# Performance work log

Hardware: AMD Instinct MI355X
Metric: run time of the kernel (lower is better)

Reference implementation:

```python
import jax, jax.numpy as jnp
import numpy as np

N = 20000      # total atoms
M = 12         # neighbors per atom
B = 41         # nbr_fea_len
ORIG = 92      # orig_atom_fea_len
F = 64         # atom_fea_len
D = 2 * F + B  # 169, gated feature width
NC = 3         # n_conv
K = 3          # k parallel gates per conv
H = 128        # h_fea_len
N0 = 400       # crystals in batch
EPS = 1e-5     # batchnorm eps


def setup_inputs() -> dict:
    key = jax.random.key(0)
    ks = jax.random.split(key, 24)
    inp = {}
    inp["atom_fea"] = jax.random.normal(ks[0], (N, ORIG), jnp.float32)
    inp["nbr_fea"] = jax.random.normal(ks[1], (N, M, B), jnp.float32)
    inp["nbr_fea_idx"] = jax.random.randint(ks[2], (N, M), 0, N)
    inp["crystal_atom_idx"] = jnp.sort(jax.random.randint(ks[3], (N,), 0, N0))
    inp["n_crystals"] = N0
    inp["emb_w"] = jax.random.normal(ks[4], (ORIG, F)) * 0.1
    inp["emb_b"] = jnp.zeros((F,), jnp.float32)
    inp["fc_w"] = jax.random.normal(ks[5], (NC, K, D, D)) * 0.05
    inp["fc_b"] = jnp.zeros((NC, K, D), jnp.float32)
    inp["bn1_g"] = jnp.ones((NC, K, D), jnp.float32)
    inp["bn1_b"] = jnp.zeros((NC, K, D), jnp.float32)
    inp["bn1_m"] = jax.random.normal(ks[6], (NC, K, D)) * 0.1
    inp["bn1_v"] = jax.random.uniform(ks[7], (NC, K, D)) * 0.5 + 0.75
    inp["bn2_g"] = jnp.ones((NC, K, F), jnp.float32)
    inp["bn2_b"] = jnp.zeros((NC, K, F), jnp.float32)
    inp["bn2_m"] = jax.random.normal(ks[8], (NC, K, F)) * 0.1
    inp["bn2_v"] = jax.random.uniform(ks[9], (NC, K, F)) * 0.5 + 0.75
    inp["atom_w"] = jax.random.normal(ks[10], (NC, K, 2 * K)) * 0.3
    inp["atom_b"] = jnp.zeros((NC, 2 * K), jnp.float32)
    inp["nbr_w"] = jax.random.normal(ks[11], (NC, K, 2 * K)) * 0.3
    inp["nbr_b"] = jnp.zeros((NC, 2 * K), jnp.float32)
    inp["fc1_w"] = jax.random.normal(ks[12], (F, H)) * 0.1
    inp["fc1_b"] = jnp.zeros((H,), jnp.float32)
    inp["out_w"] = jax.random.normal(ks[13], (H, 1)) * 0.1
    inp["out_b"] = jnp.zeros((1,), jnp.float32)
    return inp


def _conv(atom_in, nbr, idx, fc_w, fc_b, bn1_g, bn1_b, bn1_m, bn1_v,
          bn2_g, bn2_b, bn2_m, bn2_v, atom_w, atom_b, nbr_w, nbr_b):
    n, m = idx.shape
    gathered = atom_in[idx]                                   # (N,M,F) irregular gather
    self_f = jnp.broadcast_to(atom_in[:, None, :], (n, m, F))
    total = jnp.concatenate([self_f, gathered, nbr], axis=2)  # (N,M,D)
    # k parallel linear layers, vectorized over k
    g = jnp.einsum('nmd,kde->knme', total, fc_w) + fc_b[:, None, None, :]  # (K,N,M,D)
    # bn1 (eval mode, running stats)
    g = (g - bn1_m[:, None, None, :]) * jax.lax.rsqrt(bn1_v[:, None, None, :] + EPS) \
        * bn1_g[:, None, None, :] + bn1_b[:, None, None, :]
    nbr_filter = jax.nn.softmax(g[..., :F], axis=2)            # softmax over neighbors M
    nbr_core = jax.nn.relu(g[..., F:2 * F])
    new_nbr_k = g[..., 2 * F:] + nbr[None]                     # (K,N,M,B) residual on bonds
    summed = jnp.sum(nbr_filter * nbr_core, axis=2)            # (K,N,F)
    summed = (summed - bn2_m[:, None, :]) * jax.lax.rsqrt(bn2_v[:, None, :] + EPS) \
        * bn2_g[:, None, :] + bn2_b[:, None, :]
    out_k = atom_in[None] + summed                             # (K,N,F) residual on atoms
    out = jnp.moveaxis(out_k, 0, 2)                            # (N,F,K)
    new_nbr = jnp.moveaxis(new_nbr_k, 0, 3)                    # (N,M,B,K)
    og = out @ atom_w + atom_b                                 # (N,F,2K)
    ng = new_nbr @ nbr_w + nbr_b                               # (N,M,B,2K)
    out = jnp.sum(og[..., :K] * jax.nn.softmax(og[..., K:], axis=2), axis=2)
    new_nbr = jnp.sum(ng[..., :K] * jax.nn.softmax(ng[..., K:], axis=3), axis=3)
    return out, new_nbr


def reference(atom_fea, nbr_fea, nbr_fea_idx, crystal_atom_idx, n_crystals,
              emb_w, emb_b, fc_w, fc_b, bn1_g, bn1_b, bn1_m, bn1_v,
              bn2_g, bn2_b, bn2_m, bn2_v, atom_w, atom_b, nbr_w, nbr_b,
              fc1_w, fc1_b, out_w, out_b):
    x = atom_fea @ emb_w + emb_b                               # embedding
    nbr = nbr_fea
    for i in range(NC):                                        # fixed small layer loop
        x, nbr = _conv(x, nbr, nbr_fea_idx,
                       fc_w[i], fc_b[i], bn1_g[i], bn1_b[i], bn1_m[i], bn1_v[i],
                       bn2_g[i], bn2_b[i], bn2_m[i], bn2_v[i],
                       atom_w[i], atom_b[i], nbr_w[i], nbr_b[i])
    # per-crystal mean pooling via segment sum
    sums = jax.ops.segment_sum(x, crystal_atom_idx, num_segments=n_crystals)
    counts = jax.ops.segment_sum(jnp.ones((x.shape[0], 1), x.dtype),
                                 crystal_atom_idx, num_segments=n_crystals)
    crys = sums / jnp.maximum(counts, 1.0)
    crys = jax.nn.relu(crys) @ fc1_w + fc1_b
    crys = jax.nn.relu(crys)
    return crys @ out_w + out_b                                # (N0, 1)
```

## Files before the change

kernel.cpp:

```cpp
#include <hip/hip_runtime.h>
#include <math.h>

#define N_ATOMS 20000
#define M 12
#define B 41
#define ORIG 92
#define F 64
#define D 169
#define NCONV 3
#define K 3
#define TWOK 6
#define H 128
#define N0 400
#define EPS 1e-5f
#define KB (K * B)
#define NBRS 42

#define KPAD 192
#define NS 6
#define ATOMS_PER_BLK 4
#define ROWS (ATOMS_PER_BLK * 16)
#define THREADS 512
#define LFRAG 98304
#define WT_USHORTS (NCONV * 2 * LFRAG)
#define GRID (N_ATOMS / ATOMS_PER_BLK)

typedef __attribute__((ext_vector_type(8))) short bf16x8;
typedef __attribute__((ext_vector_type(4))) float f32x4;

__device__ inline unsigned short f32_to_bf16(float v) {
    unsigned int x = __float_as_uint(v);
    unsigned int r = (x + 0x7fffu + ((x >> 16) & 1u)) >> 16;
    return (unsigned short)r;
}
__device__ inline float bf16_to_f32(unsigned short u) {
    return __uint_as_float(((unsigned int)u) << 16);
}
__device__ inline unsigned int pack_hilo(float v) {
    unsigned short hi = f32_to_bf16(v);
    unsigned short lo = f32_to_bf16(v - bf16_to_f32(hi));
    return (unsigned int)hi | ((unsigned int)lo << 16);
}
__device__ inline float unpack_hilo(unsigned int p) {
    return bf16_to_f32((unsigned short)(p & 0xFFFFu)) +
           bf16_to_f32((unsigned short)(p >> 16));
}

__global__ void emb_kernel(const float* __restrict__ atom_fea,
                           const float* __restrict__ emb_w,
                           const float* __restrict__ emb_b,
                           float* __restrict__ x,
                           unsigned int* __restrict__ xp) {
    int i = blockIdx.x * blockDim.x + threadIdx.x;
    if (i >= N_ATOMS * F) return;
    int n = i / F, f = i % F;
    const float* a = atom_fea + n * ORIG;
    float acc = emb_b[f];
    #pragma unroll 4
    for (int d = 0; d < ORIG; ++d)
        acc = fmaf(a[d], emb_w[d * F + f], acc);
    x[i] = acc;
    xp[i] = pack_hilo(acc);
}

__global__ void npack_kernel(const float* __restrict__ nbr_fea,
                             unsigned int* __restrict__ nbrp) {
    int i = blockIdx.x * blockDim.x + threadIdx.x;
    if (i >= N_ATOMS * M * NBRS) return;
    int nm = i / NBRS, slot = i - nm * NBRS;
    nbrp[i] = (slot < B) ? pack_hilo(nbr_fea[nm * B + slot]) : 0u;
}

__global__ void prep_kernel(const float* __restrict__ fc_w,
                            unsigned short* __restrict__ wt) {
    int i = blockIdx.x * blockDim.x + threadIdx.x;
    if (i >= NCONV * LFRAG) return;
    int layer = i / LFRAG;
    int r = i % LFRAG;
    int s = r / 16384;
    int r2 = r % 16384;
    int c16 = r2 / 512;
    int r3 = r2 % 512;
    int lane = r3 / 8;
    int e = r3 % 8;
    int col = c16 * 16 + (lane & 15);
    int k = s * 32 + (lane >> 4) * 8 + e;
    float v = 0.f;
    if (k < D) {
        int b3 = col >> 7, cc = col & 127;
        if (b3 < 3) {
            v = fc_w[((size_t)(layer * K + b3) * D + k) * D + cc];
        } else if (cc < KB) {
            int kk = cc / B, bb = cc - kk * B;
            v = fc_w[((size_t)(layer * K + kk) * D + k) * D + 2 * F + bb];
        }
    }
    unsigned short hi = f32_to_bf16(v);
    float hf = bf16_to_f32(hi);
    unsigned short lo = f32_to_bf16(v - hf);
    size_t off = (size_t)s * 16384 + c16 * 512 + lane * 8 + e;
    wt[(size_t)(layer * 2 + 0) * LFRAG + off] = hi;
    wt[(size_t)(layer * 2 + 1) * LFRAG + off] = lo;
}

__global__ void prep2_kernel(const float* __restrict__ fc_b,
                             const float* __restrict__ bn1_g,
                             const float* __restrict__ bn1_b,
                             const float* __restrict__ bn1_m,
                             const float* __restrict__ bn1_v,
                             const float* __restrict__ bn2_g,
                             const float* __restrict__ bn2_b,
                             const float* __restrict__ bn2_m,
                             const float* __restrict__ bn2_v,
                             float* __restrict__ sc1,
                             float* __restrict__ sh1,
                             float* __restrict__ sc2,
                             float* __restrict__ sh2) {
    int i = blockIdx.x * blockDim.x + threadIdx.x;
    if (i < NCONV * K * D) {
        float sc = bn1_g[i] * rsqrtf(bn1_v[i] + EPS);
        sc1[i] = sc;
        sh1[i] = fmaf(fc_b[i], sc, bn1_b[i] - bn1_m[i] * sc);
    }
    if (i < NCONV * K * F) {
        float sc = bn2_g[i] * rsqrtf(bn2_v[i] + EPS);
        sc2[i] = sc;
        sh2[i] = bn2_b[i] - bn2_m[i] * sc;
    }
}

template <bool NEED_NBR>
__global__ __launch_bounds__(THREADS, 4)
void conv_mfma(const float* __restrict__ xin,
               const unsigned int* __restrict__ xpin,
               const unsigned int* __restrict__ nbrpin,
               const int* __restrict__ idx,
               const unsigned short* __restrict__ wtl,
               const float* __restrict__ sc1,
               const float* __restrict__ sh1,
               const float* __restrict__ sc2,
               const float* __restrict__ sh2,
               const float* __restrict__ atom_w,
               const float* __restrict__ atom_b,
               const float* __restrict__ nbr_w,
               const float* __restrict__ nbr_b,
               float* __restrict__ xout,
               unsigned int* __restrict__ xpout,
               unsigned int* __restrict__ nbrpout) {
    __shared__ unsigned short s_a[2 * ROWS * KPAD];
    __shared__ float s_sum[ATOMS_PER_BLK * K * F];

    const int t = threadIdx.x;
    const int w = t >> 6;
    const int l = t & 63;
    const int l15 = l & 15;
    const int lane3 = l >> 4;
    const int n0 = blockIdx.x * ATOMS_PER_BLK;

    {
        const int srow = t >> 3;
        const int j8 = t & 7;
        const int a = srow >> 4, m = srow & 15;
        const int n = n0 + a;
        const unsigned int mask = (unsigned int)((srow & 7) << 4);
        char* hi_base = (char*)s_a + srow * (KPAD * 2);
        char* lo_base = hi_base + 2 * ROWS * KPAD;
        if (m < M) {
            const unsigned int* xs = xpin + n * F;
            const unsigned int* xg = xpin + idx[n * M + m] * F;
            const unsigned int* nb = nbrpin + (size_t)(n * M + m) * NBRS;
            #pragma unroll
            for (int q = 0; q < 12; ++q) {
                int kp = j8 + 8 * q;
                uint2 u;
                if (kp < 32)       u = *(const uint2*)&xs[kp * 2];
                else if (kp < 64)  u = *(const uint2*)&xg[kp * 2 - 64];
                else if (kp < 85)  u = *(const uint2*)&nb[kp * 2 - 128];
                else               u = make_uint2(0u, 0u);
                unsigned int hip = (u.x & 0xFFFFu) | (u.y << 16);
                unsigned int lop = (u.x >> 16) | (u.y & 0xFFFF0000u);
                unsigned int byo = ((unsigned int)(kp * 4)) ^ mask;
                *(unsigned int*)(hi_base + byo) = hip;
                *(unsigned int*)(lo_base + byo) = lop;
            }
        } else {
            #pragma unroll
            for (int q = 0; q < 12; ++q) {
                unsigned int byo = ((unsigned int)((j8 + 8 * q) * 4)) ^ mask;
                *(unsigned int*)(hi_base + byo) = 0u;
                *(unsigned int*)(lo_base + byo) = 0u;
            }
        }
    }
    __syncthreads();

    const int kk_gate = w >> 1, half = w & 1;
    int tile[4];
    if (w < 6) {
        tile[0] = kk_gate * 8 + half * 2 + 0;
        tile[1] = kk_gate * 8 + half * 2 + 1;
        tile[2] = tile[0] + 4;
        tile[3] = tile[1] + 4;
    } else {
        tile[0] = 24 + (w - 6) * 4 + 0;
        tile[1] = 24 + (w - 6) * 4 + 1;
        tile[2] = 24 + (w - 6) * 4 + 2;
        tile[3] = 24 + (w - 6) * 4 + 3;
    }

    f32x4 acc[ATOMS_PER_BLK][4];
    #pragma unroll
    for (int a = 0; a < ATOMS_PER_BLK; ++a)
        #pragma unroll
        for (int j = 0; j < 4; ++j)
            acc[a][j] = (f32x4){0.f, 0.f, 0.f, 0.f};

    if (!(w >= 6 && !NEED_NBR)) {
        __builtin_amdgcn_s_setprio(1);
        for (int s = 0; s < NS; ++s) {
            bf16x8 ah[ATOMS_PER_BLK], al[ATOMS_PER_BLK];
            #pragma unroll
            for (int a = 0; a < ATOMS_PER_BLK; ++a) {
                int row = a * 16 + l15;
                int koff = s * 64 + lane3 * 16;
                int byte = row * (KPAD * 2) + (koff ^ ((row & 7) << 4));
                ah[a] = *reinterpret_cast<const bf16x8*>(&s_a[byte >> 1]);
                al[a] = *reinterpret_cast<const bf16x8*>(&s_a[(byte >> 1) + ROWS * KPAD]);
            }
            #pragma unroll
            for (int j = 0; j < 4; ++j) {
                const unsigned short* wp =
                    wtl + (size_t)s * 16384 + tile[j] * 512 + l * 8;
                bf16x8 bh = *reinterpret_cast<const bf16x8*>(wp);
                bf16x8 bl = *reinterpret_cast<const bf16x8*>(wp + LFRAG);
                #pragma unroll
                for (int a = 0; a < ATOMS_PER_BLK; ++a) {
                    acc[a][j] = __builtin_amdgcn_mfma_f32_16x16x32_bf16(ah[a], bh, acc[a][j], 0, 0, 0);
                    acc[a][j] = __builtin_amdgcn_mfma_f32_16x16x32_bf16(ah[a], bl, acc[a][j], 0, 0, 0);
                    acc[a][j] = __builtin_amdgcn_mfma_f32_16x16x32_bf16(al[a], bh, acc[a][j], 0, 0, 0);
                }
            }
        }
        __builtin_amdgcn_s_setprio(0);
    }
    __syncthreads();

    float* s_nnk = reinterpret_cast<float*>(s_a);

    if (w < 6) {
        const int k = kk_gate;
        #pragma unroll
        for (int a = 0; a < ATOMS_PER_BLK; ++a) {
            #pragma unroll
            for (int j = 0; j < 2; ++j) {
                int e = (half * 2 + j) * 16 + l15;
                int cf = k * D + e, cr = cf + F, c2 = k * F + e;
                float sc_f = sc1[cf], sh_f = sh1[cf];
                float sc_c = sc1[cr], sh_c = sh1[cr];
                bool act = (lane3 < 3);
                float fv[4], cv[4];
                #pragma unroll
                for (int r = 0; r < 4; ++r) {
                    fv[r] = fmaf(acc[a][j][r], sc_f, sh_f);
                    cv[r] = fmaxf(fmaf(acc[a][j + 2][r], sc_c, sh_c), 0.f);
                }
                float mx = act ? fmaxf(fmaxf(fv[0], fv[1]), fmaxf(fv[2], fv[3])) : -1e30f;
                mx = fmaxf(mx, __shfl_xor(mx, 16));
                mx = fmaxf(mx, __shfl_xor(mx, 32));
                float se = 0.f, sp = 0.f;
                #pragma unroll
                for (int r = 0; r < 4; ++r) {
                    float ex = act ? __expf(fv[r] - mx) : 0.f;
                    se += ex;
                    sp = fmaf(ex, cv[r], sp);
                }
                se += __shfl_xor(se, 16);
                se += __shfl_xor(se, 32);
                sp += __shfl_xor(sp, 16);
                sp += __shfl_xor(sp, 32);
                float summed = sp / se;
                float outv = xin[(n0 + a) * F + e] + fmaf(summed, sc2[c2], sh2[c2]);
                if (lane3 == 0) s_sum[(a * K + k) * F + e] = outv;
            }
        }
    } else if (NEED_NBR) {
        #pragma unroll
        for (int a = 0; a < ATOMS_PER_BLK; ++a) {
            #pragma unroll
            for (int j = 0; j < 4; ++j) {
                int cc = (w - 6) * 64 + j * 16 + l15;
                if (cc < KB) {
                    int kk = cc / B, bb = cc - (cc / B) * B;
                    int col = kk * D + 2 * F + bb;
                    float sc = sc1[col], sh = sh1[col];
                    #pragma unroll
                    for (int r = 0; r < 4; ++r) {
                        int m = lane3 * 4 + r;
                        if (m < M) {
                            float nv = unpack_hilo(
                                nbrpin[(size_t)((n0 + a) * M + m) * NBRS + bb]);
                            s_nnk[((a * K + kk) * M + m) * B + bb] =
                                fmaf(acc[a][j][r], sc, sh) + nv;
                        }
                    }
                }
            }
        }
    }
    __syncthreads();

    if (t < ATOMS_PER_BLK * F) {
        int a2 = t >> 6, f = t & 63;
        float og[TWOK];
        #pragma unroll
        for (int j = 0; j < TWOK; ++j) {
            float v = atom_b[j];
            #pragma unroll
            for (int q = 0; q < K; ++q)
                v = fmaf(s_sum[(a2 * K + q) * F + f], atom_w[q * TWOK + j], v);
            og[j] = v;
        }
        float mx = fmaxf(fmaxf(og[K], og[K + 1]), og[K + 2]);
        float e0 = __expf(og[K] - mx), e1 = __expf(og[K + 1] - mx), e2 = __expf(og[K + 2] - mx);
        float inv = 1.f / (e0 + e1 + e2);
        float outv = (og[0] * e0 + og[1] * e1 + og[2] * e2) * inv;
        xout[(n0 + a2) * F + f] = outv;
        xpout[(n0 + a2) * F + f] = pack_hilo(outv);
    }

    if (NEED_NBR) {
        for (int i = t; i < ATOMS_PER_BLK * M * B; i += THREADS) {
            int a2 = i / (M * B);
            int r = i - a2 * (M * B);
            int m = r / B, b = r - m * B;
            float ng[TWOK];
            #pragma unroll
            for (int j = 0; j < TWOK; ++j) {
                float v = nbr_b[j];
                #pragma unroll
                for (int q = 0; q < K; ++q)
                    v = fmaf(s_nnk[((a2 * K + q) * M + m) * B + b], nbr_w[q * TWOK + j], v);
                ng[j] = v;
            }
            float mx = fmaxf(fmaxf(ng[K], ng[K + 1]), ng[K + 2]);
            float e0 = __expf(ng[K] - mx), e1 = __expf(ng[K + 1] - mx), e2 = __expf(ng[K + 2] - mx);
            float inv = 1.f / (e0 + e1 + e2);
            float v = (ng[0] * e0 + ng[1] * e1 + ng[2] * e2) * inv;
            nbrpout[(size_t)((n0 + a2) * M + m) * NBRS + b] = pack_hilo(v);
        }
        for (int i3 = t; i3 < ATOMS_PER_BLK * M; i3 += THREADS) {
            int a2 = i3 / M, m = i3 - a2 * M;
            nbrpout[(size_t)((n0 + a2) * M + m) * NBRS + B] = 0u;
        }
    }
}

__global__ void pool_kernel(const float* __restrict__ x,
                            const int* __restrict__ cidx,
                            float* __restrict__ sums,
                            float* __restrict__ cnt) {
    int i = blockIdx.x * blockDim.x + threadIdx.x;
    if (i >= N_ATOMS * F) return;
    int n = i / F, f = i % F;
    int c = cidx[n];
    atomicAdd(&sums[c * F + f], x[i]);
    if (f == 0) atomicAdd(&cnt[c], 1.0f);
}

__global__ void head_kernel(const float* __restrict__ sums,
                            const float* __restrict__ cnt,
                            const float* __restrict__ fc1_w,
                            const float* __restrict__ fc1_b,
                            const float* __restrict__ out_w,
                            const float* __restrict__ out_b,
                            float* __restrict__ out) {
    const int c = blockIdx.x;
    const int t = threadIdx.x;
    __shared__ float a[F];
    __shared__ float red[H];
    float inv_cnt = 1.f / fmaxf(cnt[c], 1.0f);
    if (t < F) a[t] = fmaxf(sums[c * F + t] * inv_cnt, 0.f);
    __syncthreads();
    float hv = fc1_b[t];
    #pragma unroll 4
    for (int f = 0; f < F; ++f)
        hv = fmaf(a[f], fc1_w[f * H + t], hv);
    hv = fmaxf(hv, 0.f);
    red[t] = hv * out_w[t];
    __syncthreads();
    for (int s = H / 2; s > 0; s >>= 1) {
        if (t < s) red[t] += red[t + s];
        __syncthreads();
    }
    if (t == 0) out[c] = red[0] + out_b[0];
}

extern "C" void kernel_launch(void* const* d_in, const int* in_sizes, int n_in,
                              void* d_out, int out_size, void* d_ws, size_t ws_size,
                              hipStream_t stream) {
    (void)in_sizes; (void)n_in; (void)out_size; (void)ws_size;
    const float* atom_fea = (const float*)d_in[0];
    const float* nbr_fea  = (const float*)d_in[1];
    const int*   nbr_idx  = (const int*)d_in[2];
    const int*   cidx     = (const int*)d_in[3];
    const float* emb_w = (const float*)d_in[5];
    const float* emb_b = (const float*)d_in[6];
    const float* fc_w  = (const float*)d_in[7];
    const float* fc_b  = (const float*)d_in[8];
    const float* bn1_g = (const float*)d_in[9];
    const float* bn1_b = (const float*)d_in[10];
    const float* bn1_m = (const float*)d_in[11];
    const float* bn1_v = (const float*)d_in[12];
    const float* bn2_g = (const float*)d_in[13];
    const float* bn2_b = (const float*)d_in[14];
    const float* bn2_m = (const float*)d_in[15];
    const float* bn2_v = (const float*)d_in[16];
    const float* atom_w = (const float*)d_in[17];
    const float* atom_b = (const float*)d_in[18];
    const float* nbr_w  = (const float*)d_in[19];
    const float* nbr_b  = (const float*)d_in[20];
    const float* fc1_w  = (const float*)d_in[21];
    const float* fc1_b  = (const float*)d_in[22];
    const float* out_w  = (const float*)d_in[23];
    const float* out_b  = (const float*)d_in[24];
    float* out = (float*)d_out;

    float* xA   = (float*)d_ws;
    float* xB   = xA + (size_t)N_ATOMS * F;
    unsigned int* xPA = (unsigned int*)(xB + (size_t)N_ATOMS * F);
    unsigned int* xPB = xPA + (size_t)N_ATOMS * F;
    unsigned int* nbrP0 = xPB + (size_t)N_ATOMS * F;
    unsigned int* nbrPA = nbrP0 + (size_t)N_ATOMS * M * NBRS;
    float* sums = (float*)(nbrPA + (size_t)N_ATOMS * M * NBRS);
    float* cnt  = sums + (size_t)N0 * F;
    float* sc1  = cnt + N0;
    float* sh1  = sc1 + NCONV * K * D;
    float* sc2  = sh1 + NCONV * K * D;
    float* sh2  = sc2 + NCONV * K * F;
    unsigned short* wt = (unsigned short*)(sh2 + NCONV * K * F);

    prep_kernel<<<(NCONV * LFRAG + 255) / 256, 256, 0, stream>>>(fc_w, wt);
    prep2_kernel<<<(NCONV * K * D + 255) / 256, 256, 0, stream>>>(
        fc_b, bn1_g, bn1_b, bn1_m, bn1_v, bn2_g, bn2_b, bn2_m, bn2_v,
        sc1, sh1, sc2, sh2);
    npack_kernel<<<(N_ATOMS * M * NBRS + 255) / 256, 256, 0, stream>>>(nbr_fea, nbrP0);
    emb_kernel<<<(N_ATOMS * F + 255) / 256, 256, 0, stream>>>(
        atom_fea, emb_w, emb_b, xA, xPA);

    conv_mfma<true><<<GRID, THREADS, 0, stream>>>(
        xA, xPA, nbrP0, nbr_idx,
        wt, sc1, sh1, sc2, sh2,
        atom_w, atom_b, nbr_w, nbr_b, xB, xPB, nbrPA);
    conv_mfma<true><<<GRID, THREADS, 0, stream>>>(
        xB, xPB, nbrPA, nbr_idx,
        wt + (size_t)2 * LFRAG,
        sc1 + (size_t)1 * K * D, sh1 + (size_t)1 * K * D,
        sc2 + (size_t)1 * K * F, sh2 + (size_t)1 * K * F,
        atom_w + (size_t)1 * K * TWOK, atom_b + (size_t)1 * TWOK,
        nbr_w + (size_t)1 * K * TWOK, nbr_b + (size_t)1 * TWOK, xA, xPA, nbrP0);
    conv_mfma<false><<<GRID, THREADS, 0, stream>>>(
        xA, xPA, nbrP0, nbr_idx,
        wt + (size_t)4 * LFRAG,
        sc1 + (size_t)2 * K * D, sh1 + (size_t)2 * K * D,
        sc2 + (size_t)2 * K * F, sh2 + (size_t)2 * K * F,
        atom_w + (size_t)2 * K * TWOK, atom_b + (size_t)2 * TWOK,
        nbr_w + (size_t)2 * K * TWOK, nbr_b + (size_t)2 * TWOK, xB, xPB, nbrPA);

    hipMemsetAsync(sums, 0, (size_t)(N0 * F + N0) * sizeof(float), stream);
    pool_kernel<<<(N_ATOMS * F + 255) / 256, 256, 0, stream>>>(xB, cidx, sums, cnt);
    head_kernel<<<N0, H, 0, stream>>>(sums, cnt, fc1_w, fc1_b, out_w, out_b, out);
}
```

Measured before the change: 620.1 us.

## Precompute self-atom GEMM contribution per atom instead of per neighbor

Splits the gated linear layer so the self-feature part (first 64 input rows) is computed once per atom in a new pw_kernel and stored as a per-atom 512-wide buffer. The conv kernel then only multiplies the gathered neighbor and bond features (K reduced from 192 to 128) and adds the precomputed partial sums in the epilogue. This removes redundant 12x recomputation of the self term and shrinks shared memory staging. In exchange it adds an extra kernel launch per layer and writes and reads a 20000x512 float buffer, about 40 MB per layer.

```diff
diff --git a/kernel.cpp b/kernel.cpp
--- a/kernel.cpp
+++ b/kernel.cpp
@@ -16,13 +16,13 @@
 #define KB (K * B)
 #define NBRS 42
 
-#define KPAD 192
-#define NS 6
+#define KPAD 128
+#define NS 4
 #define ATOMS_PER_BLK 4
 #define ROWS (ATOMS_PER_BLK * 16)
 #define THREADS 512
-#define LFRAG 98304
-#define WT_USHORTS (NCONV * 2 * LFRAG)
+#define LFRAG_C 65536
+#define LFRAG_P 32768
 #define GRID (N_ATOMS / ATOMS_PER_BLK)
 
 typedef __attribute__((ext_vector_type(8))) short bf16x8;
@@ -44,6 +44,17 @@
 __device__ inline float unpack_hilo(unsigned int p) {
     return bf16_to_f32((unsigned short)(p & 0xFFFFu)) +
            bf16_to_f32((unsigned short)(p >> 16));
+}
+
+__device__ inline float wlookup(const float* __restrict__ fc_w,
+                                int layer, int row, int c) {
+    int b3 = c >> 7, cc = c & 127;
+    if (b3 < 3) return fc_w[((size_t)(layer * K + b3) * D + row) * D + cc];
+    if (cc < KB) {
+        int kk = cc / B, bb = cc - (cc / B) * B;
+        return fc_w[((size_t)(layer * K + kk) * D + row) * D + 2 * F + bb];
+    }
+    return 0.f;
 }
 
 __global__ void emb_kernel(const float* __restrict__ atom_fea,
@@ -71,36 +82,44 @@
     nbrp[i] = (slot < B) ? pack_hilo(nbr_fea[nm * B + slot]) : 0u;
 }
 
-__global__ void prep_kernel(const float* __restrict__ fc_w,
-                            unsigned short* __restrict__ wt) {
+__global__ void prep_c_kernel(const float* __restrict__ fc_w,
+                              unsigned short* __restrict__ wt) {
     int i = blockIdx.x * blockDim.x + threadIdx.x;
-    if (i >= NCONV * LFRAG) return;
-    int layer = i / LFRAG;
-    int r = i % LFRAG;
+    if (i >= NCONV * LFRAG_C) return;
+    int layer = i / LFRAG_C;
+    int r = i % LFRAG_C;
     int s = r / 16384;
     int r2 = r % 16384;
     int c16 = r2 / 512;
     int r3 = r2 % 512;
-    int lane = r3 / 8;
-    int e = r3 % 8;
+    int lane = r3 / 8, e = r3 % 8;
+    int col = c16 * 16 + (lane & 15);
+    int k = 64 + s * 32 + (lane >> 4) * 8 + e;
+    float v = (k < D) ? wlookup(fc_w, layer, k, col) : 0.f;
+    unsigned short hi = f32_to_bf16(v);
+    unsigned short lo = f32_to_bf16(v - bf16_to_f32(hi));
+    wt[(size_t)(layer * 2 + 0) * LFRAG_C + r] = hi;
+    wt[(size_t)(layer * 2 + 1) * LFRAG_C + r] = lo;
+}
+
+__global__ void prep_p_kernel(const float* __restrict__ fc_w,
+                              unsigned short* __restrict__ wt) {
+    int i = blockIdx.x * blockDim.x + threadIdx.x;
+    if (i >= NCONV * LFRAG_P) return;
+    int layer = i / LFRAG_P;
+    int r = i % LFRAG_P;
+    int s = r / 16384;
+    int r2 = r % 16384;
+    int c16 = r2 / 512;
+    int r3 = r2 % 512;
+    int lane = r3 / 8, e = r3 % 8;
     int col = c16 * 16 + (lane & 15);
     int k = s * 32 + (lane >> 4) * 8 + e;
-    float v = 0.f;
-    if (k < D) {
-        int b3 = col >> 7, cc = col & 127;
-        if (b3 < 3) {
-            v = fc_w[((size_t)(layer * K + b3) * D + k) * D + cc];
-        } else if (cc < KB) {
-            int kk = cc / B, bb = cc - kk * B;
-            v = fc_w[((size_t)(layer * K + kk) * D + k) * D + 2 * F + bb];
-        }
-    }
+    float v = wlookup(fc_w, layer, k, col);
     unsigned short hi = f32_to_bf16(v);
-    float hf = bf16_to_f32(hi);
-    unsigned short lo = f32_to_bf16(v - hf);
-    size_t off = (size_t)s * 16384 + c16 * 512 + lane * 8 + e;
-    wt[(size_t)(layer * 2 + 0) * LFRAG + off] = hi;
-    wt[(size_t)(layer * 2 + 1) * LFRAG + off] = lo;
+    unsigned short lo = f32_to_bf16(v - bf16_to_f32(hi));
+    wt[(size_t)(layer * 2 + 0) * LFRAG_P + r] = hi;
+    wt[(size_t)(layer * 2 + 1) * LFRAG_P + r] = lo;
 }
 
 __global__ void prep2_kernel(const float* __restrict__ fc_b,
@@ -129,6 +148,78 @@
     }
 }
 
+__global__ __launch_bounds__(512, 4)
+void pw_kernel(const unsigned int* __restrict__ xp,
+               const unsigned short* __restrict__ wtl,
+               float* __restrict__ pw) {
+    __shared__ __align__(16) unsigned short s_a[2 * 32 * 64];
+
+    const int t = threadIdx.x;
+    const int w = t >> 6, l = t & 63;
+    const int l15 = l & 15, lane3 = l >> 4;
+    const int n0 = blockIdx.x * 32;
+
+    {
+        int row = t >> 4, j16 = t & 15;
+        unsigned int mask = (unsigned int)((row & 7) << 4);
+        char* hb = (char*)s_a + row * 128;
+        const unsigned int* xr = xp + (n0 + row) * F;
+        #pragma unroll
+        for (int q = 0; q < 2; ++q) {
+            int kp = j16 + 16 * q;
+            uint2 u = *(const uint2*)&xr[kp * 2];
+            unsigned int hip = (u.x & 0xFFFFu) | (u.y << 16);
+            unsigned int lop = (u.x >> 16) | (u.y & 0xFFFF0000u);
+            unsigned int byo = ((unsigned int)(kp * 4)) ^ mask;
+            *(unsigned int*)(hb + byo) = hip;
+            *(unsigned int*)(hb + byo + 4096) = lop;
+        }
+    }
+    __syncthreads();
+
+    f32x4 acc[2][4];
+    #pragma unroll
+    for (int a = 0; a < 2; ++a)
+        #pragma unroll
+        for (int j = 0; j < 4; ++j)
+            acc[a][j] = (f32x4){0.f, 0.f, 0.f, 0.f};
+
+    #pragma unroll
+    for (int s = 0; s < 2; ++s) {
+        bf16x8 ah[2], al[2];
+        #pragma unroll
+        for (int a = 0; a < 2; ++a) {
+            int row = a * 16 + l15;
+            int byte = row * 128 + ((s * 64 + lane3 * 16) ^ ((row & 7) << 4));
+            ah[a] = *(const bf16x8*)((const char*)s_a + byte);
+            al[a] = *(const bf16x8*)((const char*)s_a + byte + 4096);
+        }
+        #pragma unroll
+        for (int j = 0; j < 4; ++j) {
+            const unsigned short* wp = wtl + s * 16384 + (w * 4 + j) * 512 + l * 8;
+            bf16x8 bh = *(const bf16x8*)wp;
+            bf16x8 bl = *(const bf16x8*)(wp + LFRAG_P);
+            #pragma unroll
+            for (int a = 0; a < 2; ++a) {
+                acc[a][j] = __builtin_amdgcn_mfma_f32_16x16x32_bf16(ah[a], bh, acc[a][j], 0, 0, 0);
+                acc[a][j] = __builtin_amdgcn_mfma_f32_16x16x32_bf16(ah[a], bl, acc[a][j], 0, 0, 0);
+                acc[a][j] = __builtin_amdgcn_mfma_f32_16x16x32_bf16(al[a], bh, acc[a][j], 0, 0, 0);
+            }
+        }
+    }
+
+    #pragma unroll
+    for (int a = 0; a < 2; ++a)
+        #pragma unroll
+        for (int j = 0; j < 4; ++j) {
+            int col = (w * 4 + j) * 16 + l15;
+            int rowb = n0 + a * 16 + lane3 * 4;
+            #pragma unroll
+            for (int r = 0; r < 4; ++r)
+                pw[(size_t)(rowb + r) * 512 + col] = acc[a][j][r];
+        }
+}
+
 template <bool NEED_NBR>
 __global__ __launch_bounds__(THREADS, 4)
 void conv_mfma(const float* __restrict__ xin,
@@ -136,6 +227,7 @@
                const unsigned int* __restrict__ nbrpin,
                const int* __restrict__ idx,
                const unsigned short* __restrict__ wtl,
+               const float* __restrict__ pw,
                const float* __restrict__ sc1,
                const float* __restrict__ sh1,
                const float* __restrict__ sc2,
@@ -166,16 +258,14 @@
         char* hi_base = (char*)s_a + srow * (KPAD * 2);
         char* lo_base = hi_base + 2 * ROWS * KPAD;
         if (m < M) {
-            const unsigned int* xs = xpin + n * F;
             const unsigned int* xg = xpin + idx[n * M + m] * F;
             const unsigned int* nb = nbrpin + (size_t)(n * M + m) * NBRS;
             #pragma unroll
-            for (int q = 0; q < 12; ++q) {
+            for (int q = 0; q < 8; ++q) {
                 int kp = j8 + 8 * q;
                 uint2 u;
-                if (kp < 32)       u = *(const uint2*)&xs[kp * 2];
-                else if (kp < 64)  u = *(const uint2*)&xg[kp * 2 - 64];
-                else if (kp < 85)  u = *(const uint2*)&nb[kp * 2 - 128];
+                if (kp < 32)       u = *(const uint2*)&xg[kp * 2];
+                else if (kp < 53)  u = *(const uint2*)&nb[(kp - 32) * 2];
                 else               u = make_uint2(0u, 0u);
                 unsigned int hip = (u.x & 0xFFFFu) | (u.y << 16);
                 unsigned int lop = (u.x >> 16) | (u.y & 0xFFFF0000u);
@@ -185,7 +275,7 @@
             }
         } else {
             #pragma unroll
-            for (int q = 0; q < 12; ++q) {
+            for (int q = 0; q < 8; ++q) {
                 unsigned int byo = ((unsigned int)((j8 + 8 * q) * 4)) ^ mask;
                 *(unsigned int*)(hi_base + byo) = 0u;
                 *(unsigned int*)(lo_base + byo) = 0u;
@@ -232,7 +322,7 @@
                 const unsigned short* wp =
                     wtl + (size_t)s * 16384 + tile[j] * 512 + l * 8;
                 bf16x8 bh = *reinterpret_cast<const bf16x8*>(wp);
-                bf16x8 bl = *reinterpret_cast<const bf16x8*>(wp + LFRAG);
+                bf16x8 bl = *reinterpret_cast<const bf16x8*>(wp + LFRAG_C);
                 #pragma unroll
                 for (int a = 0; a < ATOMS_PER_BLK; ++a) {
                     acc[a][j] = __builtin_amdgcn_mfma_f32_16x16x32_bf16(ah[a], bh, acc[a][j], 0, 0, 0);
@@ -251,9 +341,13 @@
         const int k = kk_gate;
         #pragma unroll
         for (int a = 0; a < ATOMS_PER_BLK; ++a) {
+            const float* pwl = pw + (size_t)(n0 + a) * 512;
             #pragma unroll
             for (int j = 0; j < 2; ++j) {
                 int e = (half * 2 + j) * 16 + l15;
+                int colf = tile[j] * 16 + l15;
+                float Pf = pwl[colf];
+                float Pc = pwl[colf + 64];
                 int cf = k * D + e, cr = cf + F, c2 = k * F + e;
                 float sc_f = sc1[cf], sh_f = sh1[cf];
                 float sc_c = sc1[cr], sh_c = sh1[cr];
@@ -261,8 +355,8 @@
                 float fv[4], cv[4];
                 #pragma unroll
                 for (int r = 0; r < 4; ++r) {
-                    fv[r] = fmaf(acc[a][j][r], sc_f, sh_f);
-                    cv[r] = fmaxf(fmaf(acc[a][j + 2][r], sc_c, sh_c), 0.f);
+                    fv[r] = fmaf(acc[a][j][r] + Pf, sc_f, sh_f);
+                    cv[r] = fmaxf(fmaf(acc[a][j + 2][r] + Pc, sc_c, sh_c), 0.f);
                 }
                 float mx = act ? fmaxf(fmaxf(fv[0], fv[1]), fmaxf(fv[2], fv[3])) : -1e30f;
                 mx = fmaxf(mx, __shfl_xor(mx, 16));
@@ -286,10 +380,12 @@
     } else if (NEED_NBR) {
         #pragma unroll
         for (int a = 0; a < ATOMS_PER_BLK; ++a) {
+            const float* pwl = pw + (size_t)(n0 + a) * 512;
             #pragma unroll
             for (int j = 0; j < 4; ++j) {
                 int cc = (w - 6) * 64 + j * 16 + l15;
                 if (cc < KB) {
+                    float P1 = pwl[384 + cc];
                     int kk = cc / B, bb = cc - (cc / B) * B;
                     int col = kk * D + 2 * F + bb;
                     float sc = sc1[col], sh = sh1[col];
@@ -300,7 +396,7 @@
                             float nv = unpack_hilo(
                                 nbrpin[(size_t)((n0 + a) * M + m) * NBRS + bb]);
                             s_nnk[((a * K + kk) * M + m) * B + bb] =
-                                fmaf(acc[a][j][r], sc, sh) + nv;
+                                fmaf(acc[a][j][r] + P1, sc, sh) + nv;
                         }
                     }
                 }
@@ -431,15 +527,18 @@
     unsigned int* xPB = xPA + (size_t)N_ATOMS * F;
     unsigned int* nbrP0 = xPB + (size_t)N_ATOMS * F;
     unsigned int* nbrPA = nbrP0 + (size_t)N_ATOMS * M * NBRS;
-    float* sums = (float*)(nbrPA + (size_t)N_ATOMS * M * NBRS);
+    float* pwbuf = (float*)(nbrPA + (size_t)N_ATOMS * M * NBRS);
+    float* sums = pwbuf + (size_t)N_ATOMS * 512;
     float* cnt  = sums + (size_t)N0 * F;
     float* sc1  = cnt + N0;
     float* sh1  = sc1 + NCONV * K * D;
     float* sc2  = sh1 + NCONV * K * D;
     float* sh2  = sc2 + NCONV * K * F;
-    unsigned short* wt = (unsigned short*)(sh2 + NCONV * K * F);
-
-    prep_kernel<<<(NCONV * LFRAG + 255) / 256, 256, 0, stream>>>(fc_w, wt);
+    unsigned short* wtp = (unsigned short*)(sh2 + NCONV * K * F);
+    unsigned short* wtc = wtp + (size_t)NCONV * 2 * LFRAG_P;
+
+    prep_p_kernel<<<(NCONV * LFRAG_P + 255) / 256, 256, 0, stream>>>(fc_w, wtp);
+    prep_c_kernel<<<(NCONV * LFRAG_C + 255) / 256, 256, 0, stream>>>(fc_w, wtc);
     prep2_kernel<<<(NCONV * K * D + 255) / 256, 256, 0, stream>>>(
         fc_b, bn1_g, bn1_b, bn1_m, bn1_v, bn2_g, bn2_b, bn2_m, bn2_v,
         sc1, sh1, sc2, sh2);
@@ -447,20 +546,23 @@
     emb_kernel<<<(N_ATOMS * F + 255) / 256, 256, 0, stream>>>(
         atom_fea, emb_w, emb_b, xA, xPA);
 
+    pw_kernel<<<N_ATOMS / 32, 512, 0, stream>>>(xPA, wtp, pwbuf);
     conv_mfma<true><<<GRID, THREADS, 0, stream>>>(
         xA, xPA, nbrP0, nbr_idx,
-        wt, sc1, sh1, sc2, sh2,
+        wtc, pwbuf, sc1, sh1, sc2, sh2,
         atom_w, atom_b, nbr_w, nbr_b, xB, xPB, nbrPA);
+    pw_kernel<<<N_ATOMS / 32, 512, 0, stream>>>(xPB, wtp + (size_t)2 * LFRAG_P, pwbuf);
     conv_mfma<true><<<GRID, THREADS, 0, stream>>>(
         xB, xPB, nbrPA, nbr_idx,
-        wt + (size_t)2 * LFRAG,
+        wtc + (size_t)2 * LFRAG_C, pwbuf,
         sc1 + (size_t)1 * K * D, sh1 + (size_t)1 * K * D,
         sc2 + (size_t)1 * K * F, sh2 + (size_t)1 * K * F,
         atom_w + (size_t)1 * K * TWOK, atom_b + (size_t)1 * TWOK,
         nbr_w + (size_t)1 * K * TWOK, nbr_b + (size_t)1 * TWOK, xA, xPA, nbrP0);
+    pw_kernel<<<N_ATOMS / 32, 512, 0, stream>>>(xPA, wtp + (size_t)4 * LFRAG_P, pwbuf);
     conv_mfma<false><<<GRID, THREADS, 0, stream>>>(
         xA, xPA, nbrP0, nbr_idx,
-        wt + (size_t)4 * LFRAG,
+        wtc + (size_t)4 * LFRAG_C, pwbuf,
         sc1 + (size_t)2 * K * D, sh1 + (size_t)2 * K * D,
         sc2 + (size_t)2 * K * F, sh2 + (size_t)2 * K * F,
         atom_w + (size_t)2 * K * TWOK, atom_b + (size_t)2 * TWOK,
```

After: 604.1 us, median of 2. -2.6%, faster.
